# Performance work log

Hardware: AMD Instinct MI355X
Metric: run time of the kernel (lower is better)

## Reference

```python
import jax, jax.numpy as jnp
import numpy as np

D_MODEL = 768
CODEBOOK_SIZE = 2048
CODEBOOK_DIM = 64


def setup_inputs() -> dict:
    key = jax.random.key(0)
    ks = jax.random.split(key, 10)
    B, N = 16, 4096
    h = CODEBOOK_DIM * 2  # 128
    def lin_init(k, fan_in, shape):
        bound = 1.0 / np.sqrt(fan_in)
        return jax.random.uniform(k, shape, jnp.float32, -bound, bound)
    inp = {
        "x": jax.random.normal(ks[0], (B, N, D_MODEL), jnp.float32),
        # encoder: Linear(d_model -> 2*cd), GELU, Linear(2*cd -> cd)
        "enc_w1": lin_init(ks[1], D_MODEL, (D_MODEL, h)),
        "enc_b1": lin_init(ks[2], D_MODEL, (h,)),
        "enc_w2": lin_init(ks[3], h, (h, CODEBOOK_DIM)),
        "enc_b2": lin_init(ks[4], h, (CODEBOOK_DIM,)),
        # codebook: uniform(-1/K, 1/K)
        "codebook": jax.random.uniform(ks[5], (CODEBOOK_SIZE, CODEBOOK_DIM), jnp.float32,
                                        -1.0 / CODEBOOK_SIZE, 1.0 / CODEBOOK_SIZE),
        # decoder: Linear(cd -> 2*cd), GELU, Linear(2*cd -> d_model)
        "dec_w1": lin_init(ks[6], CODEBOOK_DIM, (CODEBOOK_DIM, h)),
        "dec_b1": lin_init(ks[7], CODEBOOK_DIM, (h,)),
        "dec_w2": lin_init(ks[8], h, (h, D_MODEL)),
        "dec_b2": lin_init(ks[9], h, (D_MODEL,)),
    }
    return inp


def reference(x, enc_w1, enc_b1, enc_w2, enc_b2, codebook, dec_w1, dec_b1, dec_w2, dec_b2):
    B, N, _ = x.shape
    # encoder MLP (exact GELU, matching torch default)
    z = jax.nn.gelu(x @ enc_w1 + enc_b1, approximate=False) @ enc_w2 + enc_b2  # (B,N,cd)
    # quantize: squared-distance argmin over codebook
    flat_z = z.reshape(-1, CODEBOOK_DIM)  # (BN, cd)
    dist = (jnp.sum(flat_z * flat_z, axis=1, keepdims=True)
            + jnp.sum(codebook * codebook, axis=1)[None, :]
            - 2.0 * flat_z @ codebook.T)  # (BN, K)
    indices = jnp.argmin(dist, axis=-1)  # (BN,)
    z_q = codebook[indices].reshape(B, N, CODEBOOK_DIM)
    codebook_loss = jnp.mean((jax.lax.stop_gradient(z_q) - z) ** 2)
    embedding_loss = jnp.mean((z_q - jax.lax.stop_gradient(z)) ** 2)
    vq_loss = codebook_loss + 0.25 * embedding_loss
    # straight-through estimator
    z_q = z + jax.lax.stop_gradient(z_q - z)
    # decoder MLP
    x_rec = jax.nn.gelu(z_q @ dec_w1 + dec_b1, approximate=False) @ dec_w2 + dec_b2
    return x_rec, indices.reshape(B, N), vq_loss
```

## Files before the change

### kernel.cpp

```cpp
#include <hip/hip_runtime.h>
#include <math.h>

#define TOKENS 65536
#define DMODEL 768
#define HDIM 128
#define CDIM 64
#define NCODE 2048

__device__ __forceinline__ float gelu_exact(float v) {
    return 0.5f * v * (1.0f + erff(v * 0.7071067811865476f));
}

__device__ __forceinline__ void load_lds16(const float* g, float* l) {
    __builtin_amdgcn_global_load_lds(
        (const __attribute__((address_space(1))) void*)g,
        (__attribute__((address_space(3))) void*)l, 16, 0, 0);
}

__global__ __launch_bounds__(256) __attribute__((amdgpu_waves_per_eu(4, 4)))
void enc_fused(const float* __restrict__ x, const float* __restrict__ w1,
               const float* __restrict__ b1, const float* __restrict__ w2,
               const float* __restrict__ b2, float* __restrict__ Z)
{
    __shared__ union {
        struct { float Xs[64][32]; float Ws[32][128]; } a;
        float H1s[64][132];
    } u;

    const int t = threadIdx.x;
    const int w = t >> 6, l = t & 63;
    const size_t tok0 = (size_t)blockIdx.x * 64;
    const int tg = t >> 5;
    const int cg = t & 31;

    float acc[8][4];
    #pragma unroll
    for (int i = 0; i < 8; ++i)
        #pragma unroll
        for (int j = 0; j < 4; ++j) acc[i][j] = 0.f;

    float* XsF = &u.a.Xs[0][0];
    float* WsF = &u.a.Ws[0][0];
    const int xrow_ = l >> 3;
    const int xcol_ = 4 * (l & 7);
    const int wrow_ = l >> 5;
    const int wcol_ = 4 * (l & 31);

    for (int k0 = 0; k0 < DMODEL; k0 += 32) {
        #pragma unroll
        for (int j = 0; j < 2; ++j) {
            const int row = (w * 2 + j) * 8 + xrow_;
            load_lds16(x + (tok0 + row) * DMODEL + k0 + xcol_,
                       XsF + (w * 2 + j) * 256);
        }
        #pragma unroll
        for (int j = 0; j < 4; ++j) {
            const int row = 2 * (w * 4 + j) + wrow_;
            load_lds16(w1 + (size_t)(k0 + row) * HDIM + wcol_,
                       WsF + (w * 4 + j) * 256);
        }
        __syncthreads();
        #pragma unroll
        for (int kk = 0; kk < 32; kk += 4) {
            float4 av[8];
            #pragma unroll
            for (int i = 0; i < 8; ++i)
                av[i] = *reinterpret_cast<const float4*>(&u.a.Xs[tg + 8 * i][kk]);
            float4 bv[4];
            #pragma unroll
            for (int q = 0; q < 4; ++q)
                bv[q] = *reinterpret_cast<const float4*>(&u.a.Ws[kk + q][cg * 4]);
            #pragma unroll
            for (int i = 0; i < 8; ++i) {
                acc[i][0] = fmaf(av[i].x, bv[0].x, acc[i][0]);
                acc[i][1] = fmaf(av[i].x, bv[0].y, acc[i][1]);
                acc[i][2] = fmaf(av[i].x, bv[0].z, acc[i][2]);
                acc[i][3] = fmaf(av[i].x, bv[0].w, acc[i][3]);
                acc[i][0] = fmaf(av[i].y, bv[1].x, acc[i][0]);
                acc[i][1] = fmaf(av[i].y, bv[1].y, acc[i][1]);
                acc[i][2] = fmaf(av[i].y, bv[1].z, acc[i][2]);
                acc[i][3] = fmaf(av[i].y, bv[1].w, acc[i][3]);
                acc[i][0] = fmaf(av[i].z, bv[2].x, acc[i][0]);
                acc[i][1] = fmaf(av[i].z, bv[2].y, acc[i][1]);
                acc[i][2] = fmaf(av[i].z, bv[2].z, acc[i][2]);
                acc[i][3] = fmaf(av[i].z, bv[2].w, acc[i][3]);
                acc[i][0] = fmaf(av[i].w, bv[3].x, acc[i][0]);
                acc[i][1] = fmaf(av[i].w, bv[3].y, acc[i][1]);
                acc[i][2] = fmaf(av[i].w, bv[3].z, acc[i][2]);
                acc[i][3] = fmaf(av[i].w, bv[3].w, acc[i][3]);
            }
        }
        __syncthreads();
    }

    {
        float4 b1v = *reinterpret_cast<const float4*>(b1 + cg * 4);
        #pragma unroll
        for (int i = 0; i < 8; ++i) {
            float4 h;
            h.x = gelu_exact(acc[i][0] + b1v.x);
            h.y = gelu_exact(acc[i][1] + b1v.y);
            h.z = gelu_exact(acc[i][2] + b1v.z);
            h.w = gelu_exact(acc[i][3] + b1v.w);
            *reinterpret_cast<float4*>(&u.H1s[tg + 8 * i][cg * 4]) = h;
        }
    }
    __syncthreads();

    const int tg2 = t >> 4;
    const int cg2 = t & 15;
    const float4* w2_4 = reinterpret_cast<const float4*>(w2);
    float accB[4][4];
    #pragma unroll
    for (int i = 0; i < 4; ++i)
        #pragma unroll
        for (int j = 0; j < 4; ++j) accB[i][j] = 0.f;

    float4 bvn[4];
    #pragma unroll
    for (int q = 0; q < 4; ++q) bvn[q] = w2_4[(size_t)q * 16 + cg2];

    for (int k = 0; k < HDIM; k += 4) {
        float4 bv[4];
        #pragma unroll
        for (int q = 0; q < 4; ++q) bv[q] = bvn[q];
        if (k + 4 < HDIM) {
            #pragma unroll
            for (int q = 0; q < 4; ++q)
                bvn[q] = w2_4[(size_t)(k + 4 + q) * 16 + cg2];
        }
        float4 av[4];
        #pragma unroll
        for (int i = 0; i < 4; ++i)
            av[i] = *reinterpret_cast<const float4*>(&u.H1s[tg2 + 16 * i][k]);
        #pragma unroll
        for (int i = 0; i < 4; ++i) {
            accB[i][0] = fmaf(av[i].x, bv[0].x, accB[i][0]);
            accB[i][1] = fmaf(av[i].x, bv[0].y, accB[i][1]);
            accB[i][2] = fmaf(av[i].x, bv[0].z, accB[i][2]);
            accB[i][3] = fmaf(av[i].x, bv[0].w, accB[i][3]);
            accB[i][0] = fmaf(av[i].y, bv[1].x, accB[i][0]);
            accB[i][1] = fmaf(av[i].y, bv[1].y, accB[i][1]);
            accB[i][2] = fmaf(av[i].y, bv[1].z, accB[i][2]);
            accB[i][3] = fmaf(av[i].y, bv[1].w, accB[i][3]);
            accB[i][0] = fmaf(av[i].z, bv[2].x, accB[i][0]);
            accB[i][1] = fmaf(av[i].z, bv[2].y, accB[i][1]);
            accB[i][2] = fmaf(av[i].z, bv[2].z, accB[i][2]);
            accB[i][3] = fmaf(av[i].z, bv[2].w, accB[i][3]);
            accB[i][0] = fmaf(av[i].w, bv[3].x, accB[i][0]);
            accB[i][1] = fmaf(av[i].w, bv[3].y, accB[i][1]);
            accB[i][2] = fmaf(av[i].w, bv[3].z, accB[i][2]);
            accB[i][3] = fmaf(av[i].w, bv[3].w, accB[i][3]);
        }
    }
    {
        float4 b2v = *reinterpret_cast<const float4*>(b2 + cg2 * 4);
        #pragma unroll
        for (int i = 0; i < 4; ++i) {
            float4 o;
            o.x = accB[i][0] + b2v.x;
            o.y = accB[i][1] + b2v.y;
            o.z = accB[i][2] + b2v.z;
            o.w = accB[i][3] + b2v.w;
            *reinterpret_cast<float4*>(Z + (tok0 + tg2 + 16 * i) * CDIM + cg2 * 4) = o;
        }
    }
}

__global__ __launch_bounds__(256)
void vq_kernel(const float* __restrict__ Z, const float* __restrict__ cb,
               const float* __restrict__ cnorm, int* __restrict__ idx_out,
               float* __restrict__ idxf_out, float* __restrict__ loss_accum)
{
    __shared__ float Zs[64][68];
    __shared__ float CsT[64][128];
    __shared__ float tgsum[8];

    const int t = threadIdx.x;
    const size_t tok0 = (size_t)blockIdx.x * 64;
    const int tg = t >> 5, cg = t & 31;
    const int lc = t >> 1, lh = t & 1;

    {
        int ltok = t >> 2, lq = t & 3;
        const float4* src = reinterpret_cast<const float4*>(Z + (tok0 + ltok) * CDIM + lq * 16);
        float4* dst = reinterpret_cast<float4*>(&Zs[ltok][lq * 16]);
        dst[0] = src[0]; dst[1] = src[1]; dst[2] = src[2]; dst[3] = src[3];
    }
    float4 cv[8];
    {
        const float4* src = reinterpret_cast<const float4*>(cb + (size_t)lc * CDIM + lh * 32);
        #pragma unroll
        for (int i = 0; i < 8; ++i) cv[i] = src[i];
    }
    __syncthreads();

    float zn[8];
    {
        #pragma unroll
        for (int i = 0; i < 8; ++i) {
            float a = Zs[tg + 8 * i][cg * 2];
            float b = Zs[tg + 8 * i][cg * 2 + 1];
            zn[i] = fmaf(a, a, b * b);
        }
        #pragma unroll
        for (int m = 16; m >= 1; m >>= 1)
            #pragma unroll
            for (int i = 0; i < 8; ++i) zn[i] += __shfl_xor(zn[i], m, 32);
    }

    float minv[8]; int mini[8];
    #pragma unroll
    for (int i = 0; i < 8; ++i) { minv[i] = INFINITY; mini[i] = 0; }

    for (int tile = 0; tile < 16; ++tile) {
        const int code0 = tile * 128;
        __syncthreads();
        #pragma unroll
        for (int i = 0; i < 8; ++i) {
            int k = lh * 32 + i * 4;
            CsT[k + 0][lc] = cv[i].x;
            CsT[k + 1][lc] = cv[i].y;
            CsT[k + 2][lc] = cv[i].z;
            CsT[k + 3][lc] = cv[i].w;
        }
        __syncthreads();
        if (tile + 1 < 16) {
            const float4* src = reinterpret_cast<const float4*>(
                cb + (size_t)(code0 + 128 + lc) * CDIM + lh * 32);
            #pragma unroll
            for (int i = 0; i < 8; ++i) cv[i] = src[i];
        }

        float dot[8][4];
        #pragma unroll
        for (int i = 0; i < 8; ++i)
            #pragma unroll
            for (int j = 0; j < 4; ++j) dot[i][j] = 0.f;

        #pragma unroll
        for (int k = 0; k < CDIM; k += 4) {
            float4 av[8];
            #pragma unroll
            for (int i = 0; i < 8; ++i)
                av[i] = *reinterpret_cast<const float4*>(&Zs[tg + 8 * i][k]);
            float4 bv[4];
            #pragma unroll
            for (int q = 0; q < 4; ++q)
                bv[q] = *reinterpret_cast<const float4*>(&CsT[k + q][cg * 4]);
            #pragma unroll
            for (int i = 0; i < 8; ++i) {
                dot[i][0] = fmaf(av[i].x, bv[0].x, dot[i][0]);
                dot[i][1] = fmaf(av[i].x, bv[0].y, dot[i][1]);
                dot[i][2] = fmaf(av[i].x, bv[0].z, dot[i][2]);
                dot[i][3] = fmaf(av[i].x, bv[0].w, dot[i][3]);
                dot[i][0] = fmaf(av[i].y, bv[1].x, dot[i][0]);
                dot[i][1] = fmaf(av[i].y, bv[1].y, dot[i][1]);
                dot[i][2] = fmaf(av[i].y, bv[1].z, dot[i][2]);
                dot[i][3] = fmaf(av[i].y, bv[1].w, dot[i][3]);
                dot[i][0] = fmaf(av[i].z, bv[2].x, dot[i][0]);
                dot[i][1] = fmaf(av[i].z, bv[2].y, dot[i][1]);
                dot[i][2] = fmaf(av[i].z, bv[2].z, dot[i][2]);
                dot[i][3] = fmaf(av[i].z, bv[2].w, dot[i][3]);
                dot[i][0] = fmaf(av[i].w, bv[3].x, dot[i][0]);
                dot[i][1] = fmaf(av[i].w, bv[3].y, dot[i][1]);
                dot[i][2] = fmaf(av[i].w, bv[3].z, dot[i][2]);
                dot[i][3] = fmaf(av[i].w, bv[3].w, dot[i][3]);
            }
        }
        #pragma unroll
        for (int j = 0; j < 4; ++j) {
            int ci = code0 + cg * 4 + j;
            float cn = cnorm[ci];
            #pragma unroll
            for (int i = 0; i < 8; ++i) {
                float s = (zn[i] + cn) - 2.f * dot[i][j];
                if (s < minv[i]) { minv[i] = s; mini[i] = ci; }
            }
        }
    }

    #pragma unroll
    for (int i = 0; i < 8; ++i) {
        float v = minv[i]; int ci = mini[i];
        #pragma unroll
        for (int m = 16; m >= 1; m >>= 1) {
            float ov = __shfl_xor(v, m, 32);
            int oi = __shfl_xor(ci, m, 32);
            if (ov < v || (ov == v && oi < ci)) { v = ov; ci = oi; }
        }
        minv[i] = v; mini[i] = ci;
    }

    if (cg == 0) {
        float s = 0.f;
        #pragma unroll
        for (int i = 0; i < 8; ++i) {
            size_t tok = tok0 + tg + 8 * i;
            idx_out[tok] = mini[i];
            idxf_out[tok] = (float)mini[i];
            s += minv[i];
        }
        tgsum[tg] = s;
    }
    __syncthreads();
    if (t == 0) {
        float s = 0.f;
        #pragma unroll
        for (int i = 0; i < 8; ++i) s += tgsum[i];
        atomicAdd(loss_accum, s);
    }
}

__global__ __launch_bounds__(256)
void dec1_kernel(const float* __restrict__ cb, const float* __restrict__ w1,
                 const float* __restrict__ b1, float* __restrict__ T1,
                 float* __restrict__ cnorm)
{
    __shared__ float Cs[64][68];
    __shared__ float Ws[64][128];

    const int t = threadIdx.x;
    const int c0 = blockIdx.x * 64;
    {
        int lc = t >> 2, lq = t & 3;
        const float4* src = reinterpret_cast<const float4*>(cb + (size_t)(c0 + lc) * CDIM + lq * 16);
        float4* dst = reinterpret_cast<float4*>(&Cs[lc][lq * 16]);
        dst[0] = src[0]; dst[1] = src[1]; dst[2] = src[2]; dst[3] = src[3];
    }
    #pragma unroll
    for (int i = 0; i < 8; ++i) {
        int f = t + i * 256;
        int row = f >> 5, c4 = f & 31;
        *reinterpret_cast<float4*>(&Ws[row][c4 * 4]) =
            *reinterpret_cast<const float4*>(w1 + (size_t)row * HDIM + c4 * 4);
    }
    if (t < 64) {
        const float4* p = reinterpret_cast<const float4*>(cb + (size_t)(c0 + t) * CDIM);
        float s = 0.f;
        #pragma unroll
        for (int i = 0; i < 16; ++i) {
            float4 v = p[i];
            s = fmaf(v.x, v.x, s); s = fmaf(v.y, v.y, s);
            s = fmaf(v.z, v.z, s); s = fmaf(v.w, v.w, s);
        }
        cnorm[c0 + t] = s;
    }
    __syncthreads();
    const int tg = t >> 5, cg = t & 31;
    float acc[8][4];
    #pragma unroll
    for (int i = 0; i < 8; ++i)
        #pragma unroll
        for (int j = 0; j < 4; ++j) acc[i][j] = 0.f;
    #pragma unroll
    for (int k = 0; k < CDIM; k += 4) {
        float4 av[8];
        #pragma unroll
        for (int i = 0; i < 8; ++i)
            av[i] = *reinterpret_cast<const float4*>(&Cs[tg + 8 * i][k]);
        float4 bv[4];
        #pragma unroll
        for (int q = 0; q < 4; ++q)
            bv[q] = *reinterpret_cast<const float4*>(&Ws[k + q][cg * 4]);
        #pragma unroll
        for (int i = 0; i < 8; ++i) {
            acc[i][0] = fmaf(av[i].x, bv[0].x, acc[i][0]);
            acc[i][1] = fmaf(av[i].x, bv[0].y, acc[i][1]);
            acc[i][2] = fmaf(av[i].x, bv[0].z, acc[i][2]);
            acc[i][3] = fmaf(av[i].x, bv[0].w, acc[i][3]);
            acc[i][0] = fmaf(av[i].y, bv[1].x, acc[i][0]);
            acc[i][1] = fmaf(av[i].y, bv[1].y, acc[i][1]);
            acc[i][2] = fmaf(av[i].y, bv[1].z, acc[i][2]);
            acc[i][3] = fmaf(av[i].y, bv[1].w, acc[i][3]);
            acc[i][0] = fmaf(av[i].z, bv[2].x, acc[i][0]);
            acc[i][1] = fmaf(av[i].z, bv[2].y, acc[i][1]);
            acc[i][2] = fmaf(av[i].z, bv[2].z, acc[i][2]);
            acc[i][3] = fmaf(av[i].z, bv[2].w, acc[i][3]);
            acc[i][0] = fmaf(av[i].w, bv[3].x, acc[i][0]);
            acc[i][1] = fmaf(av[i].w, bv[3].y, acc[i][1]);
            acc[i][2] = fmaf(av[i].w, bv[3].z, acc[i][2]);
            acc[i][3] = fmaf(av[i].w, bv[3].w, acc[i][3]);
        }
    }
    float4 b1v = *reinterpret_cast<const float4*>(b1 + cg * 4);
    #pragma unroll
    for (int i = 0; i < 8; ++i) {
        float4 h;
        h.x = gelu_exact(acc[i][0] + b1v.x);
        h.y = gelu_exact(acc[i][1] + b1v.y);
        h.z = gelu_exact(acc[i][2] + b1v.z);
        h.w = gelu_exact(acc[i][3] + b1v.w);
        *reinterpret_cast<float4*>(T1 + (size_t)(c0 + tg + 8 * i) * HDIM + cg * 4) = h;
    }
}

__global__ __launch_bounds__(256)
void dec2_kernel(const float* __restrict__ T1, const float* __restrict__ w2,
                 const float* __restrict__ b2, float* __restrict__ table)
{
    __shared__ float As[64][36];
    __shared__ float Ws[32][128];
    const int t = threadIdx.x;
    const int r0 = blockIdx.x * 64;
    const int col0 = blockIdx.y * 128;
    const int tg = t >> 5, cg = t & 31;
    float acc[8][4];
    #pragma unroll
    for (int i = 0; i < 8; ++i)
        #pragma unroll
        for (int j = 0; j < 4; ++j) acc[i][j] = 0.f;

    for (int k0 = 0; k0 < HDIM; k0 += 32) {
        __syncthreads();
        {
            int lr = t >> 2, lk = t & 3;
            const float4* src = reinterpret_cast<const float4*>(T1 + (size_t)(r0 + lr) * HDIM + k0 + lk * 8);
            float4 v0 = src[0], v1 = src[1];
            float4* dst = reinterpret_cast<float4*>(&As[lr][lk * 8]);
            dst[0] = v0; dst[1] = v1;
        }
        #pragma unroll
        for (int i = 0; i < 4; ++i) {
            int f = t + i * 256;
            int row = f >> 5, c4 = f & 31;
            *reinterpret_cast<float4*>(&Ws[row][c4 * 4]) =
                *reinterpret_cast<const float4*>(w2 + (size_t)(k0 + row) * DMODEL + col0 + c4 * 4);
        }
        __syncthreads();
        #pragma unroll
        for (int kk = 0; kk < 32; kk += 4) {
            float4 av[8];
            #pragma unroll
            for (int i = 0; i < 8; ++i)
                av[i] = *reinterpret_cast<const float4*>(&As[tg + 8 * i][kk]);
            float4 bv[4];
            #pragma unroll
            for (int q = 0; q < 4; ++q)
                bv[q] = *reinterpret_cast<const float4*>(&Ws[kk + q][cg * 4]);
            #pragma unroll
            for (int i = 0; i < 8; ++i) {
                acc[i][0] = fmaf(av[i].x, bv[0].x, acc[i][0]);
                acc[i][1] = fmaf(av[i].x, bv[0].y, acc[i][1]);
                acc[i][2] = fmaf(av[i].x, bv[0].z, acc[i][2]);
                acc[i][3] = fmaf(av[i].x, bv[0].w, acc[i][3]);
                acc[i][0] = fmaf(av[i].y, bv[1].x, acc[i][0]);
                acc[i][1] = fmaf(av[i].y, bv[1].y, acc[i][1]);
                acc[i][2] = fmaf(av[i].y, bv[1].z, acc[i][2]);
                acc[i][3] = fmaf(av[i].y, bv[1].w, acc[i][3]);
                acc[i][0] = fmaf(av[i].z, bv[2].x, acc[i][0]);
                acc[i][1] = fmaf(av[i].z, bv[2].y, acc[i][1]);
                acc[i][2] = fmaf(av[i].z, bv[2].z, acc[i][2]);
                acc[i][3] = fmaf(av[i].z, bv[2].w, acc[i][3]);
                acc[i][0] = fmaf(av[i].w, bv[3].x, acc[i][0]);
                acc[i][1] = fmaf(av[i].w, bv[3].y, acc[i][1]);
                acc[i][2] = fmaf(av[i].w, bv[3].z, acc[i][2]);
                acc[i][3] = fmaf(av[i].w, bv[3].w, acc[i][3]);
            }
        }
    }
    float4 b2v = *reinterpret_cast<const float4*>(b2 + col0 + cg * 4);
    #pragma unroll
    for (int i = 0; i < 8; ++i) {
        float4 o;
        o.x = acc[i][0] + b2v.x;
        o.y = acc[i][1] + b2v.y;
        o.z = acc[i][2] + b2v.z;
        o.w = acc[i][3] + b2v.w;
        *reinterpret_cast<float4*>(table + (size_t)(r0 + tg + 8 * i) * DMODEL + col0 + cg * 4) = o;
    }
}

__global__ void gather_kernel(const float* __restrict__ table,
                              const int* __restrict__ idx, float* __restrict__ out,
                              const float* __restrict__ loss_accum,
                              float* __restrict__ loss_out)
{
    if (blockIdx.x == 0 && threadIdx.x == 0) {
        loss_out[0] = loss_accum[0] * (1.25f / 4194304.0f);
    }
    const int F = TOKENS * (DMODEL / 4);
    const float4* tab4 = reinterpret_cast<const float4*>(table);
    float4* out4 = reinterpret_cast<float4*>(out);
    for (int f = blockIdx.x * blockDim.x + threadIdx.x; f < F;
         f += gridDim.x * blockDim.x) {
        int token = f / 192;
        int j = f - token * 192;
        out4[f] = tab4[(size_t)idx[token] * 192 + j];
    }
}

extern "C" void kernel_launch(void* const* d_in, const int* in_sizes, int n_in,
                              void* d_out, int out_size, void* d_ws, size_t ws_size,
                              hipStream_t stream)
{
    const float* x      = (const float*)d_in[0];
    const float* enc_w1 = (const float*)d_in[1];
    const float* enc_b1 = (const float*)d_in[2];
    const float* enc_w2 = (const float*)d_in[3];
    const float* enc_b2 = (const float*)d_in[4];
    const float* cb     = (const float*)d_in[5];
    const float* dec_w1 = (const float*)d_in[6];
    const float* dec_b1 = (const float*)d_in[7];
    const float* dec_w2 = (const float*)d_in[8];
    const float* dec_b2 = (const float*)d_in[9];

    float* out     = (float*)d_out;
    float* xrec    = out;
    float* idxf    = out + (size_t)TOKENS * DMODEL;
    float* lossout = idxf + TOKENS;

    float* ws    = (float*)d_ws;
    float* Z     = ws;
    float* T1    = Z + (size_t)TOKENS * CDIM;
    float* table = T1 + (size_t)NCODE * HDIM;
    float* cnorm = table + (size_t)NCODE * DMODEL;
    int*   idx   = (int*)(cnorm + NCODE);
    float* lacc  = (float*)(idx + TOKENS);

    hipMemsetAsync(lacc, 0, sizeof(float), stream);

    enc_fused<<<TOKENS / 64, 256, 0, stream>>>(x, enc_w1, enc_b1, enc_w2, enc_b2, Z);
    dec1_kernel<<<NCODE / 64, 256, 0, stream>>>(cb, dec_w1, dec_b1, T1, cnorm);
    dec2_kernel<<<dim3(NCODE / 64, DMODEL / 128), 256, 0, stream>>>(T1, dec_w2, dec_b2, table);
    vq_kernel<<<TOKENS / 64, 256, 0, stream>>>(Z, cb, cnorm, idx, idxf, lacc);
    gather_kernel<<<2048, 256, 0, stream>>>(table, idx, xrec, lacc, lossout);
}
```

Measured before the change: 895.9 us.

## Load encoder X directly from global and double-buffer W1 tiles in LDS

The encoder GEMM no longer stages X tiles through LDS. Each thread now reads its 8 token rows straight from global memory as float4 values, and lanes in a half-wave share the same addresses. The W1 tile is double-buffered in LDS so the next k-slice is prefetched while the current one is used. The aim is to cut LDS traffic and hide W1 load latency behind compute. In exchange, X global-load latency is exposed inside the inner loop, with no prefetch and poor per-instruction address diversity.

```diff
diff --git a/kernel.cpp b/kernel.cpp
--- a/kernel.cpp
+++ b/kernel.cpp
@@ -23,7 +23,7 @@
                const float* __restrict__ b2, float* __restrict__ Z)
 {
     __shared__ union {
-        struct { float Xs[64][32]; float Ws[32][128]; } a;
+        float Wbuf[2][32][128];
         float H1s[64][132];
     } u;
 
@@ -39,37 +39,44 @@
         #pragma unroll
         for (int j = 0; j < 4; ++j) acc[i][j] = 0.f;
 
-    float* XsF = &u.a.Xs[0][0];
-    float* WsF = &u.a.Ws[0][0];
-    const int xrow_ = l >> 3;
-    const int xcol_ = 4 * (l & 7);
+    const float* xbase[8];
+    #pragma unroll
+    for (int i = 0; i < 8; ++i)
+        xbase[i] = x + (tok0 + tg + 8 * i) * DMODEL;
+
     const int wrow_ = l >> 5;
     const int wcol_ = 4 * (l & 31);
 
-    for (int k0 = 0; k0 < DMODEL; k0 += 32) {
-        #pragma unroll
-        for (int j = 0; j < 2; ++j) {
-            const int row = (w * 2 + j) * 8 + xrow_;
-            load_lds16(x + (tok0 + row) * DMODEL + k0 + xcol_,
-                       XsF + (w * 2 + j) * 256);
-        }
-        #pragma unroll
-        for (int j = 0; j < 4; ++j) {
-            const int row = 2 * (w * 4 + j) + wrow_;
-            load_lds16(w1 + (size_t)(k0 + row) * HDIM + wcol_,
-                       WsF + (w * 4 + j) * 256);
-        }
-        __syncthreads();
+    #define STAGE_W(buf, k0s)                                              \
+        {                                                                  \
+            float* dst = &u.Wbuf[buf][0][0];                               \
+            _Pragma("unroll")                                              \
+            for (int j = 0; j < 4; ++j) {                                  \
+                const int chunk = w * 4 + j;                               \
+                const int row = chunk * 2 + wrow_;                         \
+                load_lds16(w1 + (size_t)((k0s) + row) * HDIM + wcol_,      \
+                           dst + chunk * 256);                             \
+            }                                                              \
+        }
+
+    STAGE_W(0, 0);
+    __syncthreads();
+
+    for (int tile = 0; tile < 24; ++tile) {
+        const int k0 = tile * 32;
+        const int cur = tile & 1;
+        if (tile + 1 < 24) STAGE_W(cur ^ 1, k0 + 32);
+        const float(*Wc)[128] = u.Wbuf[cur];
         #pragma unroll
         for (int kk = 0; kk < 32; kk += 4) {
             float4 av[8];
             #pragma unroll
             for (int i = 0; i < 8; ++i)
-                av[i] = *reinterpret_cast<const float4*>(&u.a.Xs[tg + 8 * i][kk]);
+                av[i] = *reinterpret_cast<const float4*>(xbase[i] + k0 + kk);
             float4 bv[4];
             #pragma unroll
             for (int q = 0; q < 4; ++q)
-                bv[q] = *reinterpret_cast<const float4*>(&u.a.Ws[kk + q][cg * 4]);
+                bv[q] = *reinterpret_cast<const float4*>(&Wc[kk + q][cg * 4]);
             #pragma unroll
             for (int i = 0; i < 8; ++i) {
                 acc[i][0] = fmaf(av[i].x, bv[0].x, acc[i][0]);
@@ -165,6 +172,7 @@
             *reinterpret_cast<float4*>(Z + (tok0 + tg2 + 16 * i) * CDIM + cg2 * 4) = o;
         }
     }
+    #undef STAGE_W
 }
 
 __global__ __launch_bounds__(256)
```

Result: slower. 984.6 us (+9.9%).
